# Kernel tuning notes

Hardware: AMD Instinct MI355X
Metric: run time of the kernel (lower is better)

## Reference

```python
import jax, jax.numpy as jnp
import numpy as np

TOP_K = 4
ALPHA = 1.702
LIMIT = 7.0


def _glu(x):
    # interleaved gate/up split, clamp, custom swiglu
    gate = x[..., ::2]
    up = x[..., 1::2]
    gate = jnp.minimum(gate, LIMIT)
    up = jnp.clip(up, -LIMIT, LIMIT)
    glu = gate * jax.nn.sigmoid(gate * ALPHA)
    return (up + 1.0) * glu


def setup_inputs() -> dict:
    key = jax.random.key(0)
    ks = jax.random.split(key, 7)
    B, S, H, F, E = 1, 1024, 2880, 2880, 16
    w_scale = 0.02
    return {
        "hidden_states": jax.random.normal(ks[0], (B, S, H), dtype=jnp.float32),
        "router_w": jax.random.normal(ks[1], (E, H), dtype=jnp.float32) * w_scale,
        "router_b": jax.random.normal(ks[2], (E,), dtype=jnp.float32) * w_scale,
        "gate_up_w": jax.random.normal(ks[3], (E, H, 2 * F), dtype=jnp.float32) * w_scale,
        "gate_up_b": jax.random.normal(ks[4], (E, 2 * F), dtype=jnp.float32) * w_scale,
        "down_w": jax.random.normal(ks[5], (E, F, H), dtype=jnp.float32) * w_scale,
        "down_b": jax.random.normal(ks[6], (E, H), dtype=jnp.float32) * w_scale,
    }


def reference(hidden_states, router_w, router_b, gate_up_w, gate_up_b, down_w, down_b):
    B, S, H = hidden_states.shape
    x = hidden_states.reshape(-1, H)  # [T, H]
    T = x.shape[0]

    # Router: linear + top-k + softmax over top-k values, scattered to full [T, E]
    logits = x @ router_w.T + router_b  # [T, E]
    top_v, top_i = jax.lax.top_k(logits, TOP_K)  # [T, K]
    top_v = jax.nn.softmax(top_v, axis=-1)  # normalized top-k affinities
    scores = jnp.zeros_like(logits).at[jnp.arange(T)[:, None], top_i].set(top_v)  # [T, E]

    # Expert GLU MLPs (dense over experts; zero affinity masks unselected experts)
    gu = jnp.einsum('th,ehf->etf', x, gate_up_w) + gate_up_b[:, None, :]  # [E, T, 2F]
    act = _glu(gu)  # [E, T, F]
    out_e = jnp.einsum('etf,efh->eth', act, down_w) + down_b[:, None, :]  # [E, T, H]

    # Combine weighted by router scores
    out = jnp.einsum('te,eth->th', scores, out_e)  # [T, H]
    return out.reshape(B, S, H)
```

## Files before the change

### kernel.cpp

```cpp
#include <hip/hip_runtime.h>
#include <hip/hip_bf16.h>
#include <math.h>

#define H_DIM 2880
#define F_DIM 2880
#define GU_DIM 5760
#define NE 16
#define NT 1024
#define TOPK 4
#define NIT 90

typedef float f32x4 __attribute__((ext_vector_type(4)));
typedef __bf16 bf16x8 __attribute__((ext_vector_type(8)));

__device__ __forceinline__ unsigned short f2bf(float f) {
    union { float f; unsigned u; } v; v.f = f;
    return (unsigned short)((v.u + 0x8000u) >> 16);
}
__device__ __forceinline__ unsigned pk2(float a, float b) {
    return (unsigned)f2bf(a) | ((unsigned)f2bf(b) << 16);
}
__device__ __forceinline__ void gload16(const void* gsrc, void* ldst) {
    __builtin_amdgcn_global_load_lds(
        (const __attribute__((address_space(1))) unsigned int*)gsrc,
        (__attribute__((address_space(3))) unsigned int*)ldst,
        16, 0, 0);
}

__global__ __launch_bounds__(256) void castx_kernel(const float* __restrict__ x,
                                                    unsigned short* __restrict__ xb)
{
    int i = (blockIdx.x * 256 + threadIdx.x) * 8;
    float4 a = *(const float4*)(x + i);
    float4 b = *(const float4*)(x + i + 4);
    uint4 o;
    o.x = pk2(a.x, a.y); o.y = pk2(a.z, a.w);
    o.z = pk2(b.x, b.y); o.w = pk2(b.z, b.w);
    *(uint4*)(xb + i) = o;
}

__global__ __launch_bounds__(64) void router_kernel(
    const float* __restrict__ x, const float* __restrict__ rw, const float* __restrict__ rb,
    int* counts, int* topk_idx, float* topk_score)
{
    int t = blockIdx.x, lane = threadIdx.x;
    const float* xr = x + (size_t)t * H_DIM;
    float acc[NE];
#pragma unroll
    for (int e = 0; e < NE; e++) acc[e] = 0.f;
    for (int h = lane; h < H_DIM; h += 64) {
        float xv = xr[h];
#pragma unroll
        for (int e = 0; e < NE; e++) acc[e] += xv * rw[e * H_DIM + h];
    }
    float lg[NE];
#pragma unroll
    for (int e = 0; e < NE; e++) {
        float v = acc[e];
#pragma unroll
        for (int off = 32; off > 0; off >>= 1) v += __shfl_down(v, off, 64);
        lg[e] = v;
    }
    if (lane == 0) {
#pragma unroll
        for (int e = 0; e < NE; e++) lg[e] += rb[e];
        int mask = 0; float tv[TOPK]; int ti[TOPK];
        for (int k = 0; k < TOPK; k++) {
            float best = -1e30f; int bi = 0;
            for (int e = 0; e < NE; e++)
                if (!((mask >> e) & 1) && lg[e] > best) { best = lg[e]; bi = e; }
            mask |= 1 << bi; tv[k] = best; ti[k] = bi;
        }
        float m = tv[0], s = 0.f, ex[TOPK];
        for (int k = 0; k < TOPK; k++) { ex[k] = expf(tv[k] - m); s += ex[k]; }
        float inv = 1.f / s;
        for (int k = 0; k < TOPK; k++) {
            topk_idx[t * TOPK + k] = ti[k];
            topk_score[t * TOPK + k] = ex[k] * inv;
            atomicAdd(&counts[ti[k]], 1);
        }
    }
}

__global__ void offsets_kernel(const int* counts, int* offsets) {
    if (threadIdx.x == 0 && blockIdx.x == 0) {
        int s = 0;
        for (int e = 0; e < NE; e++) { offsets[e] = s; s += counts[e]; }
        offsets[NE] = s;
    }
}

__global__ void scatter_kernel(const int* topk_idx, const float* topk_score,
                               const int* offsets, int* fills, int* entry, float* entry_score,
                               int* slot_map)
{
    int t = blockIdx.x * blockDim.x + threadIdx.x;
    if (t >= NT) return;
    for (int k = 0; k < TOPK; k++) {
        int e = topk_idx[t * TOPK + k];
        int pos = atomicAdd(&fills[e], 1);
        int i = offsets[e] + pos;
        entry[i] = t | (k << 16);
        entry_score[i] = topk_score[t * TOPK + k];
        slot_map[t * TOPK + k] = i;
    }
}


#define PIPE_ISSUE(ASRC, BPTR, BSTRIDE, KK, NB, RS)                           \
    {                                                                         \
        gload16((ASRC) + (KK), &As[NB][aoff]);                                \
        RS[0] = *(const float4*)((BPTR) + (size_t)(KK) * (BSTRIDE));          \
        RS[1] = *(const float4*)((BPTR) + (size_t)((KK) + 1) * (BSTRIDE));    \
        asm volatile("" ::: "memory");                                        \
    }

#define PIPE_BWRITE(NB, RC)                                                   \
    {                                                                         \
        float4 t0_ = RC[0], t1_ = RC[1];                                      \
        *(unsigned*)&Bs[NB][bwr0] = pk2(t0_.x, t1_.x);                        \
        *(unsigned*)&Bs[NB][bwr1] = pk2(t0_.y, t1_.y);                        \
        *(unsigned*)&Bs[NB][bwr2] = pk2(t0_.z, t1_.z);                        \
        *(unsigned*)&Bs[NB][bwr3] = pk2(t0_.w, t1_.w);                        \
    }

#define PIPE_BARRIER()                                                        \
    asm volatile("s_waitcnt lgkmcnt(0)" ::: "memory");                        \
    __builtin_amdgcn_sched_barrier(0);                                        \
    __builtin_amdgcn_s_barrier();                                             \
    __builtin_amdgcn_sched_barrier(0);

#define PIPE_MFMA(CUR)                                                        \
    {                                                                         \
        bf16x8 af_[4], bq_[4];                                                \
        _Pragma("unroll") for (int i = 0; i < 4; i++)                         \
            af_[i] = *(const bf16x8*)&As[CUR][a_rd[i]];                       \
        _Pragma("unroll") for (int i = 0; i < 4; i++)                         \
            bq_[i] = *(const bf16x8*)&Bs[CUR][b_rd[i]];                       \
        _Pragma("unroll") for (int mi = 0; mi < 4; mi++)                      \
            _Pragma("unroll") for (int ni = 0; ni < 4; ni++)                  \
                acc[mi][ni] = __builtin_amdgcn_mfma_f32_16x16x32_bf16(        \
                    af_[mi], bq_[ni], acc[mi][ni], 0, 0, 0);                  \
    }

#define PIPE_BODY(ASRC, BPTR, BSTRIDE, T, CUR, NB1, NB2, RISS, RCON)          \
    {                                                                         \
        bool more_ = (T) + 2 < NIT;                                           \
        if (more_) PIPE_ISSUE(ASRC, BPTR, BSTRIDE, ((T) + 2) * 32, NB2, RISS);\
        PIPE_MFMA(CUR);                                                       \
        if ((T) + 1 < NIT) {                                                  \
            if (more_) { asm volatile("s_waitcnt vmcnt(3)" ::: "memory"); }   \
            else       { asm volatile("s_waitcnt vmcnt(0)" ::: "memory"); }   \
            PIPE_BWRITE(NB1, RCON);                                           \
            PIPE_BARRIER();                                                   \
        }                                                                     \
    }

__device__ __forceinline__ int mk_bwr(int lane, int c, int wv) {
    int n = 4 * lane + c;
    int sn = ((n >> 3) ^ (n >> 5)) & 3;
    return n * 40 + (((wv >> 2) ^ sn) * 8) + (wv & 3) * 2;
}

__global__ __launch_bounds__(1024, 1) void gemm1_kernel(
    const unsigned short* __restrict__ xb, const float* __restrict__ gw, const float* __restrict__ gb,
    const int* __restrict__ counts, const int* __restrict__ offsets,
    const int* __restrict__ entry, unsigned short* __restrict__ act)
{
    int e = blockIdx.z;
    int cnt = counts[e];
    int m0 = blockIdx.y * 256;
    if (m0 >= cnt) return;
    int n0 = blockIdx.x * 256;
    int off = offsets[e];

    __shared__ __align__(16) unsigned short As[3][256 * 32];
    __shared__ __align__(16) unsigned short Bs[3][256 * 40];
    __shared__ int toks[256];

    int tid = threadIdx.x;
    if (tid < 256) {
        int r = m0 + tid;
        toks[tid] = entry[off + (r < cnt ? r : 0)] & 0xFFFF;
    }
    __syncthreads();

    int wv = tid >> 6, lane = tid & 63;

    int ar = 16 * wv + (lane >> 2);
    int ac = lane & 3;
    const unsigned short* asrc = xb + (size_t)toks[ar] * H_DIM + 8 * (ac ^ ((ar >> 1) & 3));
    int aoff = (16 * wv) * 32;

    int bcol = n0 + 4 * lane;
    int ncc = (bcol < GU_DIM) ? bcol : (GU_DIM - 4);
    const float* bptr = gw + (size_t)e * H_DIM * GU_DIM + (size_t)(2 * wv) * GU_DIM + ncc;
    int bwr0 = mk_bwr(lane, 0, wv);
    int bwr1 = mk_bwr(lane, 1, wv);
    int bwr2 = mk_bwr(lane, 2, wv);
    int bwr3 = mk_bwr(lane, 3, wv);

    int wm = (wv & 3) * 64, wn = (wv >> 2) * 64;
    int r16 = lane & 15, q = lane >> 4;

    f32x4 acc[4][4] = {};
    int a_rd[4], b_rd[4];
#pragma unroll
    for (int i = 0; i < 4; i++) {
        int m = wm + i * 16 + r16;
        a_rd[i] = m * 32 + ((q ^ ((m >> 1) & 3)) * 8);
        int n = wn + i * 16 + r16;
        int sn = ((n >> 3) ^ (n >> 5)) & 3;
        b_rd[i] = n * 40 + ((q ^ sn) * 8);
    }

    float4 rA[2], rB[2];
    PIPE_ISSUE(asrc, bptr, GU_DIM, 0, 0, rA);
    PIPE_ISSUE(asrc, bptr, GU_DIM, 32, 1, rB);
    asm volatile("s_waitcnt vmcnt(3)" ::: "memory");
    PIPE_BWRITE(0, rA);
    PIPE_BARRIER();

    int c0 = 0;
    for (int it = 0; it < NIT; it += 2) {
        int c1 = c0 + 1; if (c1 == 3) c1 = 0;
        int c2 = c1 + 1; if (c2 == 3) c2 = 0;
        PIPE_BODY(asrc, bptr, GU_DIM, it,     c0, c1, c2, rA, rB);
        PIPE_BODY(asrc, bptr, GU_DIM, it + 1, c1, c2, c0, rB, rA);
        c0 = c2;
    }

    const float* gbp = gb + (size_t)e * GU_DIM;
#pragma unroll
    for (int ni = 0; ni < 4; ni++) {
        int col = n0 + wn + ni * 16 + r16;
        float bias = (col < GU_DIM) ? gbp[col] : 0.f;
#pragma unroll
        for (int mi = 0; mi < 4; mi++) {
#pragma unroll
            for (int r = 0; r < 4; r++) {
                float v = acc[mi][ni][r] + bias;
                float vo = __shfl_xor(v, 1, 64);
                float gate = (lane & 1) ? vo : v;
                float up   = (lane & 1) ? v  : vo;
                gate = fminf(gate, 7.0f);
                up = fminf(fmaxf(up, -7.0f), 7.0f);
                float glu = gate / (1.0f + expf(-1.702f * gate));
                float a = (up + 1.0f) * glu;
                int row = m0 + wm + mi * 16 + q * 4 + r;
                if (row < cnt && col < GU_DIM && !(lane & 1))
                    act[(size_t)(off + row) * F_DIM + (col >> 1)] = f2bf(a);
            }
        }
    }
}

__global__ __launch_bounds__(1024, 1) void gemm2_kernel(
    const unsigned short* __restrict__ act, const float* __restrict__ dw, const float* __restrict__ db,
    const int* __restrict__ counts, const int* __restrict__ offsets,
    const float* __restrict__ entry_score, float* __restrict__ slot_out)
{
    int e = blockIdx.z;
    int cnt = counts[e];
    int m0 = blockIdx.y * 256;
    if (m0 >= cnt) return;
    int n0 = blockIdx.x * 256;
    int off = offsets[e];

    __shared__ __align__(16) unsigned short As[3][256 * 32];
    __shared__ __align__(16) unsigned short Bs[3][256 * 40];
    __shared__ float scs[256];

    int tid = threadIdx.x;
    if (tid < 256) {
        int r = m0 + tid;
        scs[tid] = entry_score[off + (r < cnt ? r : 0)];
    }
    __syncthreads();

    int wv = tid >> 6, lane = tid & 63;

    int ar = 16 * wv + (lane >> 2);
    int ac = lane & 3;
    const unsigned short* asrc = act + (size_t)(off + m0 + ar) * F_DIM + 8 * (ac ^ ((ar >> 1) & 3));
    int aoff = (16 * wv) * 32;

    int bcol = n0 + 4 * lane;
    int ncc = (bcol < H_DIM) ? bcol : (H_DIM - 4);
    const float* bptr = dw + (size_t)e * F_DIM * H_DIM + (size_t)(2 * wv) * H_DIM + ncc;
    int bwr0 = mk_bwr(lane, 0, wv);
    int bwr1 = mk_bwr(lane, 1, wv);
    int bwr2 = mk_bwr(lane, 2, wv);
    int bwr3 = mk_bwr(lane, 3, wv);

    int wm = (wv & 3) * 64, wn = (wv >> 2) * 64;
    int r16 = lane & 15, q = lane >> 4;

    f32x4 acc[4][4] = {};
    int a_rd[4], b_rd[4];
#pragma unroll
    for (int i = 0; i < 4; i++) {
        int m = wm + i * 16 + r16;
        a_rd[i] = m * 32 + ((q ^ ((m >> 1) & 3)) * 8);
        int n = wn + i * 16 + r16;
        int sn = ((n >> 3) ^ (n >> 5)) & 3;
        b_rd[i] = n * 40 + ((q ^ sn) * 8);
    }

    float4 rA[2], rB[2];
    PIPE_ISSUE(asrc, bptr, H_DIM, 0, 0, rA);
    PIPE_ISSUE(asrc, bptr, H_DIM, 32, 1, rB);
    asm volatile("s_waitcnt vmcnt(3)" ::: "memory");
    PIPE_BWRITE(0, rA);
    PIPE_BARRIER();

    int c0 = 0;
    for (int it = 0; it < NIT; it += 2) {
        int c1 = c0 + 1; if (c1 == 3) c1 = 0;
        int c2 = c1 + 1; if (c2 == 3) c2 = 0;
        PIPE_BODY(asrc, bptr, H_DIM, it,     c0, c1, c2, rA, rB);
        PIPE_BODY(asrc, bptr, H_DIM, it + 1, c1, c2, c0, rB, rA);
        c0 = c2;
    }

    const float* dbp = db + (size_t)e * H_DIM;
#pragma unroll
    for (int ni = 0; ni < 4; ni++) {
        int col = n0 + wn + ni * 16 + r16;
        float bias = (col < H_DIM) ? dbp[col] : 0.f;
#pragma unroll
        for (int mi = 0; mi < 4; mi++) {
#pragma unroll
            for (int r = 0; r < 4; r++) {
                int lr = wm + mi * 16 + q * 4 + r;
                if (m0 + lr < cnt && col < H_DIM) {
                    float v = (acc[mi][ni][r] + bias) * scs[lr];
                    slot_out[(size_t)(off + m0 + lr) * H_DIM + col] = v;
                }
            }
        }
    }
}

__global__ __launch_bounds__(256) void gather_kernel(
    const float* __restrict__ slot_out, const int* __restrict__ slot_map,
    float* __restrict__ out)
{
    int t = blockIdx.x;
    int s0 = slot_map[t * TOPK + 0];
    int s1 = slot_map[t * TOPK + 1];
    int s2 = slot_map[t * TOPK + 2];
    int s3 = slot_map[t * TOPK + 3];
    const float* r0 = slot_out + (size_t)s0 * H_DIM;
    const float* r1 = slot_out + (size_t)s1 * H_DIM;
    const float* r2 = slot_out + (size_t)s2 * H_DIM;
    const float* r3 = slot_out + (size_t)s3 * H_DIM;
    float* op = out + (size_t)t * H_DIM;
    for (int h = threadIdx.x * 4; h < H_DIM; h += 1024) {
        f32x4 v = *(const f32x4*)(r0 + h) + *(const f32x4*)(r1 + h)
                + *(const f32x4*)(r2 + h) + *(const f32x4*)(r3 + h);
        *(f32x4*)(op + h) = v;
    }
}

extern "C" void kernel_launch(void* const* d_in, const int* in_sizes, int n_in,
                              void* d_out, int out_size, void* d_ws, size_t ws_size,
                              hipStream_t stream)
{
    const float* x  = (const float*)d_in[0];
    const float* rw = (const float*)d_in[1];
    const float* rb = (const float*)d_in[2];
    const float* gw = (const float*)d_in[3];
    const float* gb = (const float*)d_in[4];
    const float* dw = (const float*)d_in[5];
    const float* db = (const float*)d_in[6];
    float* out = (float*)d_out;

    char* ws = (char*)d_ws;
    int*   counts      = (int*)(ws);
    int*   fills       = (int*)(ws + 64);
    int*   offsets     = (int*)(ws + 128);
    int*   topk_idx    = (int*)(ws + 256);
    float* topk_score  = (float*)(ws + 16640);
    int*   entry       = (int*)(ws + 33024);
    float* entry_score = (float*)(ws + 49408);
    int*   slot_map    = (int*)(ws + 65792);
    unsigned short* act = (unsigned short*)(ws + 131072);
    unsigned short* xb  = (unsigned short*)(ws + 25198592);
    float* slot_out     = (float*)(ws + 31096832);

    hipMemsetAsync(ws, 0, 256, stream);

    castx_kernel<<<1440, 256, 0, stream>>>(x, xb);
    router_kernel<<<NT, 64, 0, stream>>>(x, rw, rb, counts, topk_idx, topk_score);
    offsets_kernel<<<1, 32, 0, stream>>>(counts, offsets);
    scatter_kernel<<<4, 256, 0, stream>>>(topk_idx, topk_score, offsets, fills, entry, entry_score, slot_map);
    gemm1_kernel<<<dim3(23, 4, NE), 1024, 0, stream>>>(xb, gw, gb, counts, offsets, entry, act);
    gemm2_kernel<<<dim3(12, 4, NE), 1024, 0, stream>>>(act, dw, db, counts, offsets, entry_score, slot_out);
    gather_kernel<<<NT, 256, 0, stream>>>(slot_out, slot_map, out);
}
```

Measured before the change: 2.118 ms.

## Double-buffer GEMM main loop with K=64 steps and one barrier per step

Replaces the three-stage, K=32-per-step software pipeline in both expert GEMMs with a two-buffer scheme that loads and computes K=64 per step as two 32-wide halves. This halves the number of workgroup barriers and LDS write phases per tile. In exchange, each step waits for all outstanding loads (vmcnt(0)) before the next LDS write, so the prefetch lookahead shrinks from two stages to one. Per-thread staging registers double.

New measurement: 2.135 ms. Within noise of the previous version (+0.8%).

```diff
diff --git a/kernel.cpp b/kernel.cpp
--- a/kernel.cpp
+++ b/kernel.cpp
@@ -8,7 +8,7 @@
 #define NE 16
 #define NT 1024
 #define TOPK 4
-#define NIT 90
+#define NIT2 45
 
 typedef float f32x4 __attribute__((ext_vector_type(4)));
 typedef __bf16 bf16x8 __attribute__((ext_vector_type(8)));
@@ -107,60 +107,53 @@
 }
 
 
-#define PIPE_ISSUE(ASRC, BPTR, BSTRIDE, KK, NB, RS)                           \
+__device__ __forceinline__ int mk_bwr(int lane, int c, int wv) {
+    int n = 4 * lane + c;
+    int sn = ((n >> 3) ^ (n >> 5)) & 3;
+    return n * 40 + (((wv >> 2) ^ sn) * 8) + (wv & 3) * 2;
+}
+
+#define GEMM_MFMA_HALF(AP, BP)                                                \
     {                                                                         \
-        gload16((ASRC) + (KK), &As[NB][aoff]);                                \
-        RS[0] = *(const float4*)((BPTR) + (size_t)(KK) * (BSTRIDE));          \
-        RS[1] = *(const float4*)((BPTR) + (size_t)((KK) + 1) * (BSTRIDE));    \
+        bf16x8 af_[4], bq_[4];                                                \
+        _Pragma("unroll") for (int i = 0; i < 4; i++)                         \
+            af_[i] = *(const bf16x8*)&(AP)[a_rd[i]];                          \
+        _Pragma("unroll") for (int i = 0; i < 4; i++)                         \
+            bq_[i] = *(const bf16x8*)&(BP)[b_rd[i]];                          \
+        _Pragma("unroll") for (int mi = 0; mi < 4; mi++)                      \
+            _Pragma("unroll") for (int ni = 0; ni < 4; ni++)                  \
+                acc[mi][ni] = __builtin_amdgcn_mfma_f32_16x16x32_bf16(        \
+                    af_[mi], bq_[ni], acc[mi][ni], 0, 0, 0);                  \
+    }
+
+#define GEMM_ISSUE(BUF, KK)                                                   \
+    {                                                                         \
+        gload16(asrc + (KK), &As[BUF][0][aoff]);                              \
+        gload16(asrc + (KK) + 32, &As[BUF][1][aoff]);                         \
+        r0[0] = *(const float4*)(bp + (size_t)(KK) * bstride);                \
+        r0[1] = *(const float4*)(bp + (size_t)((KK) + 1) * bstride);          \
+        r1[0] = *(const float4*)(bp + (size_t)((KK) + 32) * bstride);         \
+        r1[1] = *(const float4*)(bp + (size_t)((KK) + 33) * bstride);         \
         asm volatile("" ::: "memory");                                        \
     }
 
-#define PIPE_BWRITE(NB, RC)                                                   \
+#define GEMM_BWRITE(BUF)                                                      \
     {                                                                         \
-        float4 t0_ = RC[0], t1_ = RC[1];                                      \
-        *(unsigned*)&Bs[NB][bwr0] = pk2(t0_.x, t1_.x);                        \
-        *(unsigned*)&Bs[NB][bwr1] = pk2(t0_.y, t1_.y);                        \
-        *(unsigned*)&Bs[NB][bwr2] = pk2(t0_.z, t1_.z);                        \
-        *(unsigned*)&Bs[NB][bwr3] = pk2(t0_.w, t1_.w);                        \
-    }
-
-#define PIPE_BARRIER()                                                        \
+        *(unsigned*)&Bs[BUF][0][bwr0] = pk2(r0[0].x, r0[1].x);                \
+        *(unsigned*)&Bs[BUF][0][bwr1] = pk2(r0[0].y, r0[1].y);                \
+        *(unsigned*)&Bs[BUF][0][bwr2] = pk2(r0[0].z, r0[1].z);                \
+        *(unsigned*)&Bs[BUF][0][bwr3] = pk2(r0[0].w, r0[1].w);                \
+        *(unsigned*)&Bs[BUF][1][bwr0] = pk2(r1[0].x, r1[1].x);                \
+        *(unsigned*)&Bs[BUF][1][bwr1] = pk2(r1[0].y, r1[1].y);                \
+        *(unsigned*)&Bs[BUF][1][bwr2] = pk2(r1[0].z, r1[1].z);                \
+        *(unsigned*)&Bs[BUF][1][bwr3] = pk2(r1[0].w, r1[1].w);                \
+    }
+
+#define GEMM_BARRIER()                                                        \
     asm volatile("s_waitcnt lgkmcnt(0)" ::: "memory");                        \
     __builtin_amdgcn_sched_barrier(0);                                        \
     __builtin_amdgcn_s_barrier();                                             \
     __builtin_amdgcn_sched_barrier(0);
-
-#define PIPE_MFMA(CUR)                                                        \
-    {                                                                         \
-        bf16x8 af_[4], bq_[4];                                                \
-        _Pragma("unroll") for (int i = 0; i < 4; i++)                         \
-            af_[i] = *(const bf16x8*)&As[CUR][a_rd[i]];                       \
-        _Pragma("unroll") for (int i = 0; i < 4; i++)                         \
-            bq_[i] = *(const bf16x8*)&Bs[CUR][b_rd[i]];                       \
-        _Pragma("unroll") for (int mi = 0; mi < 4; mi++)                      \
-            _Pragma("unroll") for (int ni = 0; ni < 4; ni++)                  \
-                acc[mi][ni] = __builtin_amdgcn_mfma_f32_16x16x32_bf16(        \
-                    af_[mi], bq_[ni], acc[mi][ni], 0, 0, 0);                  \
-    }
-
-#define PIPE_BODY(ASRC, BPTR, BSTRIDE, T, CUR, NB1, NB2, RISS, RCON)          \
-    {                                                                         \
-        bool more_ = (T) + 2 < NIT;                                           \
-        if (more_) PIPE_ISSUE(ASRC, BPTR, BSTRIDE, ((T) + 2) * 32, NB2, RISS);\
-        PIPE_MFMA(CUR);                                                       \
-        if ((T) + 1 < NIT) {                                                  \
-            if (more_) { asm volatile("s_waitcnt vmcnt(3)" ::: "memory"); }   \
-            else       { asm volatile("s_waitcnt vmcnt(0)" ::: "memory"); }   \
-            PIPE_BWRITE(NB1, RCON);                                           \
-            PIPE_BARRIER();                                                   \
-        }                                                                     \
-    }
-
-__device__ __forceinline__ int mk_bwr(int lane, int c, int wv) {
-    int n = 4 * lane + c;
-    int sn = ((n >> 3) ^ (n >> 5)) & 3;
-    return n * 40 + (((wv >> 2) ^ sn) * 8) + (wv & 3) * 2;
-}
 
 __global__ __launch_bounds__(1024, 1) void gemm1_kernel(
     const unsigned short* __restrict__ xb, const float* __restrict__ gw, const float* __restrict__ gb,
@@ -174,8 +167,8 @@
     int n0 = blockIdx.x * 256;
     int off = offsets[e];
 
-    __shared__ __align__(16) unsigned short As[3][256 * 32];
-    __shared__ __align__(16) unsigned short Bs[3][256 * 40];
+    __shared__ __align__(16) unsigned short As[2][2][256 * 32];
+    __shared__ __align__(16) unsigned short Bs[2][2][256 * 40];
     __shared__ int toks[256];
 
     int tid = threadIdx.x;
@@ -194,7 +187,8 @@
 
     int bcol = n0 + 4 * lane;
     int ncc = (bcol < GU_DIM) ? bcol : (GU_DIM - 4);
-    const float* bptr = gw + (size_t)e * H_DIM * GU_DIM + (size_t)(2 * wv) * GU_DIM + ncc;
+    const float* bp = gw + (size_t)e * H_DIM * GU_DIM + (size_t)(2 * wv) * GU_DIM + ncc;
+    const size_t bstride = GU_DIM;
     int bwr0 = mk_bwr(lane, 0, wv);
     int bwr1 = mk_bwr(lane, 1, wv);
     int bwr2 = mk_bwr(lane, 2, wv);
@@ -214,20 +208,25 @@
         b_rd[i] = n * 40 + ((q ^ sn) * 8);
     }
 
-    float4 rA[2], rB[2];
-    PIPE_ISSUE(asrc, bptr, GU_DIM, 0, 0, rA);
-    PIPE_ISSUE(asrc, bptr, GU_DIM, 32, 1, rB);
-    asm volatile("s_waitcnt vmcnt(3)" ::: "memory");
-    PIPE_BWRITE(0, rA);
-    PIPE_BARRIER();
-
-    int c0 = 0;
-    for (int it = 0; it < NIT; it += 2) {
-        int c1 = c0 + 1; if (c1 == 3) c1 = 0;
-        int c2 = c1 + 1; if (c2 == 3) c2 = 0;
-        PIPE_BODY(asrc, bptr, GU_DIM, it,     c0, c1, c2, rA, rB);
-        PIPE_BODY(asrc, bptr, GU_DIM, it + 1, c1, c2, c0, rB, rA);
-        c0 = c2;
+    float4 r0[2], r1[2];
+    GEMM_ISSUE(0, 0);
+    asm volatile("s_waitcnt vmcnt(0)" ::: "memory");
+    __builtin_amdgcn_sched_barrier(0);
+    GEMM_BWRITE(0);
+    GEMM_BARRIER();
+
+    for (int t = 0; t < NIT2; t++) {
+        int cur = t & 1, nxt = cur ^ 1;
+        bool more = (t + 1 < NIT2);
+        if (more) GEMM_ISSUE(nxt, (t + 1) * 64);
+        GEMM_MFMA_HALF(As[cur][0], Bs[cur][0]);
+        GEMM_MFMA_HALF(As[cur][1], Bs[cur][1]);
+        if (more) {
+            asm volatile("s_waitcnt vmcnt(0)" ::: "memory");
+            __builtin_amdgcn_sched_barrier(0);
+            GEMM_BWRITE(nxt);
+            GEMM_BARRIER();
+        }
     }
 
     const float* gbp = gb + (size_t)e * GU_DIM;
@@ -267,8 +266,8 @@
     int n0 = blockIdx.x * 256;
     int off = offsets[e];
 
-    __shared__ __align__(16) unsigned short As[3][256 * 32];
-    __shared__ __align__(16) unsigned short Bs[3][256 * 40];
+    __shared__ __align__(16) unsigned short As[2][2][256 * 32];
+    __shared__ __align__(16) unsigned short Bs[2][2][256 * 40];
     __shared__ float scs[256];
 
     int tid = threadIdx.x;
@@ -287,7 +286,8 @@
 
     int bcol = n0 + 4 * lane;
     int ncc = (bcol < H_DIM) ? bcol : (H_DIM - 4);
-    const float* bptr = dw + (size_t)e * F_DIM * H_DIM + (size_t)(2 * wv) * H_DIM + ncc;
+    const float* bp = dw + (size_t)e * F_DIM * H_DIM + (size_t)(2 * wv) * H_DIM + ncc;
+    const size_t bstride = H_DIM;
     int bwr0 = mk_bwr(lane, 0, wv);
     int bwr1 = mk_bwr(lane, 1, wv);
     int bwr2 = mk_bwr(lane, 2, wv);
@@ -307,20 +307,25 @@
         b_rd[i] = n * 40 + ((q ^ sn) * 8);
     }
 
-    float4 rA[2], rB[2];
-    PIPE_ISSUE(asrc, bptr, H_DIM, 0, 0, rA);
-    PIPE_ISSUE(asrc, bptr, H_DIM, 32, 1, rB);
-    asm volatile("s_waitcnt vmcnt(3)" ::: "memory");
-    PIPE_BWRITE(0, rA);
-    PIPE_BARRIER();
-
-    int c0 = 0;
-    for (int it = 0; it < NIT; it += 2) {
-        int c1 = c0 + 1; if (c1 == 3) c1 = 0;
-        int c2 = c1 + 1; if (c2 == 3) c2 = 0;
-        PIPE_BODY(asrc, bptr, H_DIM, it,     c0, c1, c2, rA, rB);
-        PIPE_BODY(asrc, bptr, H_DIM, it + 1, c1, c2, c0, rB, rA);
-        c0 = c2;
+    float4 r0[2], r1[2];
+    GEMM_ISSUE(0, 0);
+    asm volatile("s_waitcnt vmcnt(0)" ::: "memory");
+    __builtin_amdgcn_sched_barrier(0);
+    GEMM_BWRITE(0);
+    GEMM_BARRIER();
+
+    for (int t = 0; t < NIT2; t++) {
+        int cur = t & 1, nxt = cur ^ 1;
+        bool more = (t + 1 < NIT2);
+        if (more) GEMM_ISSUE(nxt, (t + 1) * 64);
+        GEMM_MFMA_HALF(As[cur][0], Bs[cur][0]);
+        GEMM_MFMA_HALF(As[cur][1], Bs[cur][1]);
+        if (more) {
+            asm volatile("s_waitcnt vmcnt(0)" ::: "memory");
+            __builtin_amdgcn_sched_barrier(0);
+            GEMM_BWRITE(nxt);
+            GEMM_BARRIER();
+        }
     }
 
     const float* dbp = db + (size_t)e * H_DIM;
```
